# Performance work log

Hardware: AMD Instinct MI355X
Metric: run time of the kernel (lower is better)

The kernel has to match this reference:

```python
import jax, jax.numpy as jnp
import numpy as np

EMBED_DIM = 1024
NUM_HEADS = 16
HEAD_DIM = EMBED_DIM // NUM_HEADS


def setup_inputs() -> dict:
    key = jax.random.key(0)
    ks = jax.random.split(key, 12)
    B, S, D = 4, 2048, EMBED_DIM
    scale = 1.0 / np.sqrt(D)
    inp = {
        "query": jax.random.normal(ks[0], (B, S, D), jnp.float32),
        "key": jax.random.normal(ks[1], (B, S, D), jnp.float32),
        "value": jax.random.normal(ks[2], (B, S, D), jnp.float32),
        # nn.Linear weights: [out_features, in_features], y = x @ W.T + b
        "Wq": jax.random.normal(ks[3], (D, D), jnp.float32) * scale,
        "bq": jnp.zeros((D,), jnp.float32),
        "Wk": jax.random.normal(ks[4], (D, D), jnp.float32) * scale,
        "bk": jnp.zeros((D,), jnp.float32),
        "Wv": jax.random.normal(ks[5], (D, D), jnp.float32) * scale,
        "bv": jnp.zeros((D,), jnp.float32),
        "Wo": jax.random.normal(ks[6], (D, D), jnp.float32) * scale,
        "bo": jnp.zeros((D,), jnp.float32),
    }
    return inp


def reference(query, key, value, Wq, bq, Wk, bk, Wv, bv, Wo, bo):
    B, Sq, D = query.shape
    Sk = key.shape[1]
    H, Dh = NUM_HEADS, HEAD_DIM

    def proj(x, W, b):
        # [B,S,D] -> [B,H,S,Dh]
        y = jnp.einsum('bsd,ed->bse', x, W) + b
        return y.reshape(x.shape[0], x.shape[1], H, Dh).transpose(0, 2, 1, 3)

    q = proj(query, Wq, bq)
    k = proj(key, Wk, bk)
    v = proj(value, Wv, bv)

    # sigmoid attention (no softmax); dropout is identity in eval mode
    scores = jnp.einsum('bhqd,bhkd->bhqk', q, k) / jnp.sqrt(jnp.float32(Dh)).astype(q.dtype)
    attn = jax.nn.sigmoid(scores)
    out = jnp.einsum('bhqk,bhkd->bhqd', attn, v)

    out = out.transpose(0, 2, 1, 3).reshape(B, Sq, D)
    return jnp.einsum('bsd,ed->bse', out, Wo) + bo
```

## Files before the change

### kernel.cpp

```cpp
#include <hip/hip_runtime.h>


typedef _Float16 f16x2 __attribute__((ext_vector_type(2)));
typedef _Float16 f16x4 __attribute__((ext_vector_type(4)));
typedef _Float16 f16x8 __attribute__((ext_vector_type(8)));
typedef __fp16   h16x2 __attribute__((ext_vector_type(2)));
typedef float    f32x4 __attribute__((ext_vector_type(4)));
typedef float    f32x16 __attribute__((ext_vector_type(16)));

typedef __attribute__((address_space(3))) void* lds_vp;
typedef const __attribute__((address_space(1))) void* gbl_vp;

__device__ __forceinline__ void gld_lds16(const void* g, void* l) {
  __builtin_amdgcn_global_load_lds((gbl_vp)g, (lds_vp)l, 16, 0, 0);
}

__device__ __forceinline__ f16x8 cvt8(float4 a, float4 b) {
  return (f16x8){(_Float16)a.x, (_Float16)a.y, (_Float16)a.z, (_Float16)a.w,
                 (_Float16)b.x, (_Float16)b.y, (_Float16)b.z, (_Float16)b.w};
}

__device__ __forceinline__ f16x2 pk2(float a, float b) {
  h16x2 r = __builtin_amdgcn_cvt_pkrtz(a, b);
  return __builtin_bit_cast(f16x2, r);
}

__device__ __forceinline__ float exp2_fast(float x) {
#if __has_builtin(__builtin_amdgcn_exp2f)
  return __builtin_amdgcn_exp2f(x);
#else
  float r;
  asm("v_exp_f32 %0, %1" : "=v"(r) : "v"(x));
  return r;
#endif
}

#define BM 128
#define BN 128
#define BK 32

template <bool AF16, bool BF16, bool TRANSV, bool OUTF32, bool SWZ>
__global__ __launch_bounds__(256) void gemm_bt(const void* __restrict__ Av,
                                               const void* __restrict__ Bv,
                                               const float* __restrict__ bias,
                                               void* __restrict__ Yv,
                                               int M, int N, int K) {
  __shared__ __align__(16) _Float16 sA[BM * BK];
  __shared__ __align__(16) _Float16 sB[BN * BK];

  const int t = threadIdx.x, lane = t & 63, wid = t >> 6;
  int m0, n0;
  if constexpr (SWZ) {
    const int li = (int)(blockIdx.x + 64 * blockIdx.y);
    const int mb = (li & 7) * 8 + ((li >> 3) & 7);
    const int nb = li >> 6;
    m0 = mb * BM; n0 = nb * BN;
  } else {
    m0 = blockIdx.x * BM; n0 = blockIdx.y * BN;
  }
  const int wm = (wid >> 1) * 64, wn = (wid & 1) * 64;
  const int lrow = lane & 15, g = lane >> 4;

  f32x4 acc[4][4] = {};

  const int arow = 16 * wid + (lane >> 2);
  const int gq = (lane & 3) ^ ((lane >> 3) & 3);
  _Float16* lA1 = sA + wid * 512;
  _Float16* lA2 = sA + 2048 + wid * 512;
  _Float16* lB1 = sB + wid * 512;
  _Float16* lB2 = sB + 2048 + wid * 512;

  const int mrow = t >> 1, mhalf = t & 1;
  const int mm = (mrow >> 1) & 3;
  const int ch_lo = mrow * 4 + ((2 * mhalf) ^ mm);
  const int ch_hi = ch_lo ^ 1;

  const _Float16* pA16a = nullptr; const _Float16* pA16b = nullptr;
  const float* pA32 = nullptr;
  if constexpr (AF16) {
    const _Float16* A = (const _Float16*)Av;
    pA16a = A + (size_t)(m0 + arow) * K + gq * 8;
    pA16b = A + (size_t)(m0 + 64 + arow) * K + gq * 8;
  } else {
    pA32 = (const float*)Av + (size_t)(m0 + mrow) * K + mhalf * 16;
  }
  const _Float16* pB16a = nullptr; const _Float16* pB16b = nullptr;
  const float* pB32 = nullptr;
  if constexpr (BF16) {
    const _Float16* B = (const _Float16*)Bv;
    pB16a = B + (size_t)(n0 + arow) * K + gq * 8;
    pB16b = B + (size_t)(n0 + 64 + arow) * K + gq * 8;
  } else {
    pB32 = (const float*)Bv + (size_t)(n0 + mrow) * K + mhalf * 16;
  }

  const int xr = g ^ ((lrow >> 1) & 3);

  for (int k0 = 0; k0 < K; k0 += BK) {
    float4 av[4], bv4[4];
    if constexpr (!AF16) {
      const float4* p = (const float4*)(pA32 + k0);
      av[0] = p[0]; av[1] = p[1]; av[2] = p[2]; av[3] = p[3];
    }
    if constexpr (!BF16) {
      const float4* p = (const float4*)(pB32 + k0);
      bv4[0] = p[0]; bv4[1] = p[1]; bv4[2] = p[2]; bv4[3] = p[3];
    }
    __syncthreads();
    if constexpr (AF16) {
      gld_lds16(pA16a + k0, lA1);
      gld_lds16(pA16b + k0, lA2);
    } else {
      *(f16x8*)(sA + ch_lo * 8) = cvt8(av[0], av[1]);
      *(f16x8*)(sA + ch_hi * 8) = cvt8(av[2], av[3]);
    }
    if constexpr (BF16) {
      gld_lds16(pB16a + k0, lB1);
      gld_lds16(pB16b + k0, lB2);
    } else {
      *(f16x8*)(sB + ch_lo * 8) = cvt8(bv4[0], bv4[1]);
      *(f16x8*)(sB + ch_hi * 8) = cvt8(bv4[2], bv4[3]);
    }
    __syncthreads();

    f16x8 af[4], bf[4];
#pragma unroll
    for (int i = 0; i < 4; i++)
      af[i] = *(const f16x8*)(sA + (wm + i * 16 + lrow) * 32 + xr * 8);
#pragma unroll
    for (int j = 0; j < 4; j++)
      bf[j] = *(const f16x8*)(sB + (wn + j * 16 + lrow) * 32 + xr * 8);
#pragma unroll
    for (int i = 0; i < 4; i++)
#pragma unroll
      for (int j = 0; j < 4; j++)
        acc[i][j] = __builtin_amdgcn_mfma_f32_16x16x32_f16(af[i], bf[j], acc[i][j], 0, 0, 0);
  }

  const int orow = g * 4, ocol = lrow;
#pragma unroll
  for (int j = 0; j < 4; j++) {
    const int col = n0 + wn + j * 16 + ocol;
    const float bv = bias[col];
#pragma unroll
    for (int i = 0; i < 4; i++) {
      const int row = m0 + wm + i * 16 + orow;
      if constexpr (TRANSV) {
        _Float16* VT = (_Float16*)Yv;
        int s = row & 2047;
        int sp = (s & ~12) | ((s & 4) << 1) | ((s & 8) >> 1);
        _Float16* dst = VT + (((size_t)(row >> 11) * 16 + (col >> 6)) * 64 + (col & 63)) * 2048 + sp;
        f16x4 v = {(_Float16)(acc[i][j][0] + bv), (_Float16)(acc[i][j][1] + bv),
                   (_Float16)(acc[i][j][2] + bv), (_Float16)(acc[i][j][3] + bv)};
        *(f16x4*)dst = v;
      } else if constexpr (OUTF32) {
        float* Y = (float*)Yv;
#pragma unroll
        for (int r = 0; r < 4; r++) Y[(size_t)(row + r) * N + col] = acc[i][j][r] + bv;
      } else {
        _Float16* Y = (_Float16*)Yv;
#pragma unroll
        for (int r = 0; r < 4; r++) Y[(size_t)(row + r) * N + col] = (_Float16)(acc[i][j][r] + bv);
      }
    }
  }
}

__global__ __launch_bounds__(256) void qkv_gemm(const _Float16* __restrict__ Xq,
                                                const _Float16* __restrict__ Xk,
                                                const _Float16* __restrict__ Xv,
                                                const _Float16* __restrict__ W,
                                                const float* __restrict__ bq,
                                                const float* __restrict__ bk,
                                                const float* __restrict__ bv,
                                                _Float16* __restrict__ Qo,
                                                _Float16* __restrict__ Ko,
                                                _Float16* __restrict__ VT) {
  __shared__ __align__(16) _Float16 sA[BM * BK];
  __shared__ __align__(16) _Float16 sB[BN * BK];

  const int t = threadIdx.x, lane = t & 63, wid = t >> 6;
  const int li = (int)(blockIdx.x + 24 * blockIdx.y);
  const int xcol = li >> 6;
  const int mb = (li & 7) * 8 + ((li >> 3) & 7);
  const int n0g = xcol * BN, m0 = mb * BM;
  const int seg = xcol >> 3, n0 = n0g & 1023;
  const _Float16* A = (seg == 0) ? Xq : (seg == 1) ? Xk : Xv;
  const float* bias = (seg == 0) ? bq : (seg == 1) ? bk : bv;
  const int K = 1024;

  const int wm = (wid >> 1) * 64, wn = (wid & 1) * 64;
  const int lrow = lane & 15, g = lane >> 4;

  f32x4 acc[4][4] = {};

  const int arow = 16 * wid + (lane >> 2);
  const int gq = (lane & 3) ^ ((lane >> 3) & 3);
  _Float16* lA1 = sA + wid * 512;
  _Float16* lA2 = sA + 2048 + wid * 512;
  _Float16* lB1 = sB + wid * 512;
  _Float16* lB2 = sB + 2048 + wid * 512;

  const _Float16* pA16a = A + (size_t)(m0 + arow) * K + gq * 8;
  const _Float16* pA16b = A + (size_t)(m0 + 64 + arow) * K + gq * 8;
  const _Float16* pB16a = W + (size_t)(n0g + arow) * K + gq * 8;
  const _Float16* pB16b = W + (size_t)(n0g + 64 + arow) * K + gq * 8;

  const int xr = g ^ ((lrow >> 1) & 3);

  for (int k0 = 0; k0 < K; k0 += BK) {
    __syncthreads();
    gld_lds16(pA16a + k0, lA1);
    gld_lds16(pA16b + k0, lA2);
    gld_lds16(pB16a + k0, lB1);
    gld_lds16(pB16b + k0, lB2);
    __syncthreads();

    f16x8 af[4], bf[4];
#pragma unroll
    for (int i = 0; i < 4; i++)
      af[i] = *(const f16x8*)(sA + (wm + i * 16 + lrow) * 32 + xr * 8);
#pragma unroll
    for (int j = 0; j < 4; j++)
      bf[j] = *(const f16x8*)(sB + (wn + j * 16 + lrow) * 32 + xr * 8);
#pragma unroll
    for (int i = 0; i < 4; i++)
#pragma unroll
      for (int j = 0; j < 4; j++)
        acc[i][j] = __builtin_amdgcn_mfma_f32_16x16x32_f16(af[i], bf[j], acc[i][j], 0, 0, 0);
  }

  const int orow = g * 4, ocol = lrow;
#pragma unroll
  for (int j = 0; j < 4; j++) {
    const int col = n0 + wn + j * 16 + ocol;
    const float bvv = bias[col];
#pragma unroll
    for (int i = 0; i < 4; i++) {
      const int row = m0 + wm + i * 16 + orow;
      if (seg == 2) {
        int s = row & 2047;
        int sp = (s & ~12) | ((s & 4) << 1) | ((s & 8) >> 1);
        _Float16* dst = VT + (((size_t)(row >> 11) * 16 + (col >> 6)) * 64 + (col & 63)) * 2048 + sp;
        f16x4 v = {(_Float16)(acc[i][j][0] + bvv), (_Float16)(acc[i][j][1] + bvv),
                   (_Float16)(acc[i][j][2] + bvv), (_Float16)(acc[i][j][3] + bvv)};
        *(f16x4*)dst = v;
      } else {
        _Float16* Y = (seg == 0) ? Qo : Ko;
#pragma unroll
        for (int r = 0; r < 4; r++) Y[(size_t)(row + r) * 1024 + col] = (_Float16)(acc[i][j][r] + bvv);
      }
    }
  }
}

#define LDS_ROW 72
#define TILE_E (64 * LDS_ROW)

__global__ __launch_bounds__(256, 2) void attn_sig(const _Float16* __restrict__ Q,
                                                   const _Float16* __restrict__ K,
                                                   const _Float16* __restrict__ VT,
                                                   _Float16* __restrict__ O) {
  __shared__ __align__(16) _Float16 smem[4 * TILE_E];

  const int t = threadIdx.x, lane = t & 63, wid = t >> 6;
  const int l31 = lane & 31, g5 = lane >> 5;
  const int li = (int)(blockIdx.x + 8 * blockIdx.y + 128 * blockIdx.z);
  const int swz = (li & 7) * 64 + (li >> 3);
  const int qb = swz & 7, hb = swz >> 3;
  const int h = hb & 15, b = hb >> 4;
  const int q0 = qb * 256;
  const int qw = q0 + wid * 64;
  const int NT = 32;

  f16x8 qf0[4], qf1[4];
  {
    const _Float16* qp = Q + (size_t)(b * 2048 + qw + l31) * 1024 + h * 64;
#pragma unroll
    for (int dhc = 0; dhc < 4; dhc++) {
      qf0[dhc] = *(const f16x8*)(qp + dhc * 16 + g5 * 8) * (_Float16)-0.18033688f;
      qf1[dhc] = *(const f16x8*)(qp + 32 * 1024 + dhc * 16 + g5 * 8) * (_Float16)-0.18033688f;
    }
  }

  f32x16 oacc00 = {}, oacc01 = {}, oacc10 = {}, oacc11 = {};

  const int srow = t >> 2, scol = (t & 3) * 16;
  const _Float16* kbase = K + ((size_t)(b * 2048) + srow) * 1024 + h * 64 + scol;
  const _Float16* vbase = VT + ((size_t)((b * 16 + h) * 64 + srow)) * 2048 + scol;

#define LOAD_TILE(tile)                                                  \
  ka = *(const uint4*)(kbase + (size_t)(tile) * 64 * 1024);              \
  kb = *(const uint4*)(kbase + (size_t)(tile) * 64 * 1024 + 8);          \
  va = *(const uint4*)(vbase + (tile) * 64);                             \
  vb = *(const uint4*)(vbase + (tile) * 64 + 8);

#define WRITE_TILE(p)                                                    \
  {                                                                      \
    _Float16* dK = smem + (p) * 2 * TILE_E;                              \
    _Float16* dV = dK + TILE_E;                                          \
    *(uint4*)&dK[srow * LDS_ROW + scol] = ka;                            \
    *(uint4*)&dK[srow * LDS_ROW + scol + 8] = kb;                        \
    *(uint4*)&dV[srow * LDS_ROW + scol] = va;                            \
    *(uint4*)&dV[srow * LDS_ROW + scol + 8] = vb;                        \
  }

#define PACK_PF(pf, sacc)                                                \
  {                                                                      \
    _Pragma("unroll")                                                    \
    for (int G = 0; G < 2; G++) {                                        \
      union { f16x8 v; f16x2 hh[4]; } u;                                 \
      _Pragma("unroll")                                                  \
      for (int pr = 0; pr < 4; pr++) {                                   \
        float e0 = exp2_fast(sacc[G * 8 + pr * 2 + 0]);                  \
        float e1 = exp2_fast(sacc[G * 8 + pr * 2 + 1]);                  \
        u.hh[pr] = pk2(__builtin_amdgcn_rcpf(1.0f + e0),                 \
                       __builtin_amdgcn_rcpf(1.0f + e1));                \
      }                                                                  \
      pf[G] = u.v;                                                       \
    }                                                                    \
  }

#define CHUNK(c)                                                                      \
  {                                                                                   \
    const _Float16* sk_ = sKp + ((c) * 32 + l31) * LDS_ROW + g5 * 8;                  \
    f16x8 kf0 = *(const f16x8*)(sk_ + 0);                                             \
    f16x8 kf1 = *(const f16x8*)(sk_ + 16);                                            \
    f16x8 kf2 = *(const f16x8*)(sk_ + 32);                                            \
    f16x8 kf3 = *(const f16x8*)(sk_ + 48);                                            \
    f32x16 s0 = {}, s1 = {};                                                          \
    __builtin_amdgcn_s_setprio(1);                                                    \
    s0 = __builtin_amdgcn_mfma_f32_32x32x16_f16(kf0, qf0[0], s0, 0, 0, 0);            \
    s1 = __builtin_amdgcn_mfma_f32_32x32x16_f16(kf0, qf1[0], s1, 0, 0, 0);            \
    s0 = __builtin_amdgcn_mfma_f32_32x32x16_f16(kf1, qf0[1], s0, 0, 0, 0);            \
    s1 = __builtin_amdgcn_mfma_f32_32x32x16_f16(kf1, qf1[1], s1, 0, 0, 0);            \
    s0 = __builtin_amdgcn_mfma_f32_32x32x16_f16(kf2, qf0[2], s0, 0, 0, 0);            \
    s1 = __builtin_amdgcn_mfma_f32_32x32x16_f16(kf2, qf1[2], s1, 0, 0, 0);            \
    s0 = __builtin_amdgcn_mfma_f32_32x32x16_f16(kf3, qf0[3], s0, 0, 0, 0);            \
    s1 = __builtin_amdgcn_mfma_f32_32x32x16_f16(kf3, qf1[3], s1, 0, 0, 0);            \
    __builtin_amdgcn_s_setprio(0);                                                    \
    f16x8 pf0[2], pf1[2];                                                             \
    PACK_PF(pf0, s0);                                                                 \
    PACK_PF(pf1, s1);                                                                 \
    const _Float16* sv_ = sVp + l31 * LDS_ROW + (c) * 32 + g5 * 8;                    \
    f16x8 vf00 = *(const f16x8*)(sv_ + 0);                                            \
    f16x8 vf01 = *(const f16x8*)(sv_ + 16);                                           \
    f16x8 vf10 = *(const f16x8*)(sv_ + 32 * LDS_ROW);                                 \
    f16x8 vf11 = *(const f16x8*)(sv_ + 32 * LDS_ROW + 16);                            \
    __builtin_amdgcn_s_setprio(1);                                                    \
    oacc00 = __builtin_amdgcn_mfma_f32_32x32x16_f16(vf00, pf0[0], oacc00, 0, 0, 0);   \
    oacc10 = __builtin_amdgcn_mfma_f32_32x32x16_f16(vf00, pf1[0], oacc10, 0, 0, 0);   \
    oacc01 = __builtin_amdgcn_mfma_f32_32x32x16_f16(vf10, pf0[0], oacc01, 0, 0, 0);   \
    oacc11 = __builtin_amdgcn_mfma_f32_32x32x16_f16(vf10, pf1[0], oacc11, 0, 0, 0);   \
    oacc00 = __builtin_amdgcn_mfma_f32_32x32x16_f16(vf01, pf0[1], oacc00, 0, 0, 0);   \
    oacc10 = __builtin_amdgcn_mfma_f32_32x32x16_f16(vf01, pf1[1], oacc10, 0, 0, 0);   \
    oacc01 = __builtin_amdgcn_mfma_f32_32x32x16_f16(vf11, pf0[1], oacc01, 0, 0, 0);   \
    oacc11 = __builtin_amdgcn_mfma_f32_32x32x16_f16(vf11, pf1[1], oacc11, 0, 0, 0);   \
    __builtin_amdgcn_s_setprio(0);                                                    \
  }

  uint4 ka, kb, va, vb;

  LOAD_TILE(0);
  WRITE_TILE(0);
  LOAD_TILE(1);

  for (int tt = 0; tt < NT; ++tt) {
    const int p = tt & 1;
    const _Float16* sKp = smem + p * 2 * TILE_E;
    const _Float16* sVp = sKp + TILE_E;
    __syncthreads();
    if (tt + 1 < NT) { WRITE_TILE(p ^ 1); }
    if (tt + 2 < NT) { LOAD_TILE(tt + 2); }
    CHUNK(0);
    CHUNK(1);
  }

  _Float16* ep = smem;
#pragma unroll
  for (int pass = 0; pass < 2; pass++) {
    __syncthreads();
    if ((wid >> 1) == pass) {
      const int rbase = (wid & 1) * 64;
#pragma unroll
      for (int c = 0; c < 4; c++) {
        f16x4 a0 = {(_Float16)oacc00[4 * c + 0], (_Float16)oacc00[4 * c + 1],
                    (_Float16)oacc00[4 * c + 2], (_Float16)oacc00[4 * c + 3]};
        f16x4 a1 = {(_Float16)oacc01[4 * c + 0], (_Float16)oacc01[4 * c + 1],
                    (_Float16)oacc01[4 * c + 2], (_Float16)oacc01[4 * c + 3]};
        *(f16x4*)&ep[(rbase + l31) * LDS_ROW + 0 * 32 + c * 8 + g5 * 4] = a0;
        *(f16x4*)&ep[(rbase + l31) * LDS_ROW + 1 * 32 + c * 8 + g5 * 4] = a1;
        f16x4 b0 = {(_Float16)oacc10[4 * c + 0], (_Float16)oacc10[4 * c + 1],
                    (_Float16)oacc10[4 * c + 2], (_Float16)oacc10[4 * c + 3]};
        f16x4 b1 = {(_Float16)oacc11[4 * c + 0], (_Float16)oacc11[4 * c + 1],
                    (_Float16)oacc11[4 * c + 2], (_Float16)oacc11[4 * c + 3]};
        *(f16x4*)&ep[(rbase + 32 + l31) * LDS_ROW + 0 * 32 + c * 8 + g5 * 4] = b0;
        *(f16x4*)&ep[(rbase + 32 + l31) * LDS_ROW + 1 * 32 + c * 8 + g5 * 4] = b1;
      }
    }
    __syncthreads();
#pragma unroll
    for (int i = 0; i < 4; i++) {
      const int q = i * 32 + (t >> 3), dhc = t & 7;
      f16x8 row = *(const f16x8*)&ep[q * LDS_ROW + dhc * 8];
      *(f16x8*)(O + (size_t)(b * 2048 + q0 + pass * 128 + q) * 1024 + h * 64 + dhc * 8) = row;
    }
  }
#undef LOAD_TILE
#undef WRITE_TILE
#undef PACK_PF
#undef CHUNK
}

struct CvtArgs {
  const float* src[7];
  _Float16* dst[7];
  int n[7];
  int cnt;
};

__global__ __launch_bounds__(256) void cvt_f32_f16(CvtArgs a) {
  const int ti = blockIdx.y;
  if (ti >= a.cnt) return;
  const int i = (blockIdx.x * 256 + threadIdx.x) * 8;
  if (i >= a.n[ti]) return;
  const float4* s = (const float4*)(a.src[ti] + i);
  float4 x = s[0], y = s[1];
  *(f16x8*)(a.dst[ti] + i) = cvt8(x, y);
}

extern "C" void kernel_launch(void* const* d_in, const int* in_sizes, int n_in,
                              void* d_out, int out_size, void* d_ws, size_t ws_size,
                              hipStream_t stream) {
  const float* query = (const float*)d_in[0];
  const float* key   = (const float*)d_in[1];
  const float* value = (const float*)d_in[2];
  const float* Wq = (const float*)d_in[3];
  const float* bq = (const float*)d_in[4];
  const float* Wk = (const float*)d_in[5];
  const float* bk = (const float*)d_in[6];
  const float* Wv = (const float*)d_in[7];
  const float* bv = (const float*)d_in[8];
  const float* Wo = (const float*)d_in[9];
  const float* bo = (const float*)d_in[10];
  float* out = (float*)d_out;

  const int D = 1024, M = 8192;
  const size_t MB = 1024 * 1024;
  char* ws = (char*)d_ws;
  dim3 bb(256);

  if (ws_size >= 104 * MB) {
    _Float16* Xq = (_Float16*)(ws + 0 * MB);
    _Float16* Xk = (_Float16*)(ws + 16 * MB);
    _Float16* Xv = (_Float16*)(ws + 32 * MB);
    _Float16* Qp = (_Float16*)(ws + 48 * MB);
    _Float16* Kp = (_Float16*)(ws + 64 * MB);
    _Float16* VT = (_Float16*)(ws + 80 * MB);
    _Float16* Wf = (_Float16*)(ws + 96 * MB);
    _Float16* AO = Xq;
    CvtArgs ca{};
    ca.src[0] = query; ca.dst[0] = Xq; ca.n[0] = M * D;
    ca.src[1] = key;   ca.dst[1] = Xk; ca.n[1] = M * D;
    ca.src[2] = value; ca.dst[2] = Xv; ca.n[2] = M * D;
    ca.src[3] = Wq; ca.dst[3] = Wf + 0 * 1048576; ca.n[3] = D * D;
    ca.src[4] = Wk; ca.dst[4] = Wf + 1 * 1048576; ca.n[4] = D * D;
    ca.src[5] = Wv; ca.dst[5] = Wf + 2 * 1048576; ca.n[5] = D * D;
    ca.src[6] = Wo; ca.dst[6] = Wf + 3 * 1048576; ca.n[6] = D * D;
    ca.cnt = 7;
    cvt_f32_f16<<<dim3(4096, 7), bb, 0, stream>>>(ca);
    qkv_gemm<<<dim3(24, 64), bb, 0, stream>>>(Xq, Xk, Xv, Wf, bq, bk, bv, Qp, Kp, VT);
    attn_sig<<<dim3(8, 16, 4), bb, 0, stream>>>(Qp, Kp, VT, AO);
    gemm_bt<true, true, false, true, true><<<dim3(64, 8), bb, 0, stream>>>(AO, Wf + 3 * 1048576, bo, out, M, D, D);
  } else {
    _Float16* Qp = (_Float16*)(ws + 0 * MB);
    _Float16* Kp = (_Float16*)(ws + 16 * MB);
    _Float16* VT = (_Float16*)(ws + 32 * MB);
    _Float16* AO = (_Float16*)(ws + 48 * MB);
    gemm_bt<false, false, false, false, false><<<dim3(64, 8), bb, 0, stream>>>(query, Wq, bq, Qp, M, D, D);
    gemm_bt<false, false, false, false, false><<<dim3(64, 8), bb, 0, stream>>>(key,   Wk, bk, Kp, M, D, D);
    gemm_bt<false, false, true,  false, false><<<dim3(64, 8), bb, 0, stream>>>(value, Wv, bv, VT, M, D, D);
    attn_sig<<<dim3(8, 16, 4), bb, 0, stream>>>(Qp, Kp, VT, AO);
    gemm_bt<true, false, false, true, false><<<dim3(64, 8), bb, 0, stream>>>(AO, Wo, bo, out, M, D, D);
  }
}
```

Baseline: 349.6 us.

## Double GEMM K-tile to 64, fold Q scale into Wq conversion, flatten cvt grid

```diff
diff --git a/kernel.cpp b/kernel.cpp
--- a/kernel.cpp
+++ b/kernel.cpp
@@ -10,6 +10,8 @@
 
 typedef __attribute__((address_space(3))) void* lds_vp;
 typedef const __attribute__((address_space(1))) void* gbl_vp;
+
+#define QSCALE -0.18033688f
 
 __device__ __forceinline__ void gld_lds16(const void* g, void* l) {
   __builtin_amdgcn_global_load_lds((gbl_vp)g, (lds_vp)l, 16, 0, 0);
@@ -37,7 +39,7 @@
 
 #define BM 128
 #define BN 128
-#define BK 32
+#define BK 64
 
 template <bool AF16, bool BF16, bool TRANSV, bool OUTF32, bool SWZ>
 __global__ __launch_bounds__(256) void gemm_bt(const void* __restrict__ Av,
@@ -63,78 +65,78 @@
 
   f32x4 acc[4][4] = {};
 
-  const int arow = 16 * wid + (lane >> 2);
-  const int gq = (lane & 3) ^ ((lane >> 3) & 3);
-  _Float16* lA1 = sA + wid * 512;
-  _Float16* lA2 = sA + 2048 + wid * 512;
-  _Float16* lB1 = sB + wid * 512;
-  _Float16* lB2 = sB + 2048 + wid * 512;
+  const int srow8 = wid * 8 + (lane >> 3);
+  const int sgq = ((lane & 7) ^ (lane >> 3)) * 8;
 
   const int mrow = t >> 1, mhalf = t & 1;
-  const int mm = (mrow >> 1) & 3;
-  const int ch_lo = mrow * 4 + ((2 * mhalf) ^ mm);
-  const int ch_hi = ch_lo ^ 1;
-
-  const _Float16* pA16a = nullptr; const _Float16* pA16b = nullptr;
+
+  const _Float16* pAa = nullptr;
   const float* pA32 = nullptr;
   if constexpr (AF16) {
-    const _Float16* A = (const _Float16*)Av;
-    pA16a = A + (size_t)(m0 + arow) * K + gq * 8;
-    pA16b = A + (size_t)(m0 + 64 + arow) * K + gq * 8;
+    pAa = (const _Float16*)Av + (size_t)(m0 + srow8) * K + sgq;
   } else {
-    pA32 = (const float*)Av + (size_t)(m0 + mrow) * K + mhalf * 16;
-  }
-  const _Float16* pB16a = nullptr; const _Float16* pB16b = nullptr;
+    pA32 = (const float*)Av + (size_t)(m0 + mrow) * K + mhalf * 32;
+  }
+  const _Float16* pBa = nullptr;
   const float* pB32 = nullptr;
   if constexpr (BF16) {
-    const _Float16* B = (const _Float16*)Bv;
-    pB16a = B + (size_t)(n0 + arow) * K + gq * 8;
-    pB16b = B + (size_t)(n0 + 64 + arow) * K + gq * 8;
+    pBa = (const _Float16*)Bv + (size_t)(n0 + srow8) * K + sgq;
   } else {
-    pB32 = (const float*)Bv + (size_t)(n0 + mrow) * K + mhalf * 16;
-  }
-
-  const int xr = g ^ ((lrow >> 1) & 3);
+    pB32 = (const float*)Bv + (size_t)(n0 + mrow) * K + mhalf * 32;
+  }
 
   for (int k0 = 0; k0 < K; k0 += BK) {
-    float4 av[4], bv4[4];
+    float4 av[8], bv8[8];
     if constexpr (!AF16) {
       const float4* p = (const float4*)(pA32 + k0);
-      av[0] = p[0]; av[1] = p[1]; av[2] = p[2]; av[3] = p[3];
+#pragma unroll
+      for (int q = 0; q < 8; q++) av[q] = p[q];
     }
     if constexpr (!BF16) {
       const float4* p = (const float4*)(pB32 + k0);
-      bv4[0] = p[0]; bv4[1] = p[1]; bv4[2] = p[2]; bv4[3] = p[3];
+#pragma unroll
+      for (int q = 0; q < 8; q++) bv8[q] = p[q];
     }
     __syncthreads();
     if constexpr (AF16) {
-      gld_lds16(pA16a + k0, lA1);
-      gld_lds16(pA16b + k0, lA2);
+#pragma unroll
+      for (int i = 0; i < 4; i++)
+        gld_lds16(pAa + (size_t)i * 32 * K + k0, sA + i * 2048 + wid * 512);
     } else {
-      *(f16x8*)(sA + ch_lo * 8) = cvt8(av[0], av[1]);
-      *(f16x8*)(sA + ch_hi * 8) = cvt8(av[2], av[3]);
+#pragma unroll
+      for (int q = 0; q < 4; q++) {
+        const int glog = mhalf * 4 + q;
+        *(f16x8*)(sA + mrow * 64 + (glog ^ (mrow & 7)) * 8) = cvt8(av[2 * q], av[2 * q + 1]);
+      }
     }
     if constexpr (BF16) {
-      gld_lds16(pB16a + k0, lB1);
-      gld_lds16(pB16b + k0, lB2);
+#pragma unroll
+      for (int i = 0; i < 4; i++)
+        gld_lds16(pBa + (size_t)i * 32 * K + k0, sB + i * 2048 + wid * 512);
     } else {
-      *(f16x8*)(sB + ch_lo * 8) = cvt8(bv4[0], bv4[1]);
-      *(f16x8*)(sB + ch_hi * 8) = cvt8(bv4[2], bv4[3]);
-    }
-    __syncthreads();
-
-    f16x8 af[4], bf[4];
-#pragma unroll
-    for (int i = 0; i < 4; i++)
-      af[i] = *(const f16x8*)(sA + (wm + i * 16 + lrow) * 32 + xr * 8);
-#pragma unroll
-    for (int j = 0; j < 4; j++)
-      bf[j] = *(const f16x8*)(sB + (wn + j * 16 + lrow) * 32 + xr * 8);
-#pragma unroll
-    for (int i = 0; i < 4; i++)
+#pragma unroll
+      for (int q = 0; q < 4; q++) {
+        const int glog = mhalf * 4 + q;
+        *(f16x8*)(sB + mrow * 64 + (glog ^ (mrow & 7)) * 8) = cvt8(bv8[2 * q], bv8[2 * q + 1]);
+      }
+    }
+    __syncthreads();
+
+#pragma unroll
+    for (int kc = 0; kc < 2; kc++) {
+      f16x8 af[4], bf[4];
+#pragma unroll
+      for (int i = 0; i < 4; i++)
+        af[i] = *(const f16x8*)(sA + (wm + i * 16 + lrow) * 64 + ((kc * 4 + g) ^ (lrow & 7)) * 8);
 #pragma unroll
       for (int j = 0; j < 4; j++)
-        acc[i][j] = __builtin_amdgcn_mfma_f32_16x16x32_f16(af[i], bf[j], acc[i][j], 0, 0, 0);
+        bf[j] = *(const f16x8*)(sB + (wn + j * 16 + lrow) * 64 + ((kc * 4 + g) ^ (lrow & 7)) * 8);
+#pragma unroll
+      for (int i = 0; i < 4; i++)
+#pragma unroll
+        for (int j = 0; j < 4; j++)
+          acc[i][j] = __builtin_amdgcn_mfma_f32_16x16x32_f16(af[i], bf[j], acc[i][j], 0, 0, 0);
+    }
   }
 
   const int orow = g * 4, ocol = lrow;
@@ -187,6 +189,7 @@
   const int seg = xcol >> 3, n0 = n0g & 1023;
   const _Float16* A = (seg == 0) ? Xq : (seg == 1) ? Xk : Xv;
   const float* bias = (seg == 0) ? bq : (seg == 1) ? bk : bv;
+  const float bscale = (seg == 0) ? QSCALE : 1.0f;
   const int K = 1024;
 
   const int wm = (wid >> 1) * 64, wn = (wid & 1) * 64;
@@ -194,47 +197,44 @@
 
   f32x4 acc[4][4] = {};
 
-  const int arow = 16 * wid + (lane >> 2);
-  const int gq = (lane & 3) ^ ((lane >> 3) & 3);
-  _Float16* lA1 = sA + wid * 512;
-  _Float16* lA2 = sA + 2048 + wid * 512;
-  _Float16* lB1 = sB + wid * 512;
-  _Float16* lB2 = sB + 2048 + wid * 512;
-
-  const _Float16* pA16a = A + (size_t)(m0 + arow) * K + gq * 8;
-  const _Float16* pA16b = A + (size_t)(m0 + 64 + arow) * K + gq * 8;
-  const _Float16* pB16a = W + (size_t)(n0g + arow) * K + gq * 8;
-  const _Float16* pB16b = W + (size_t)(n0g + 64 + arow) * K + gq * 8;
-
-  const int xr = g ^ ((lrow >> 1) & 3);
+  const int srow8 = wid * 8 + (lane >> 3);
+  const int sgq = ((lane & 7) ^ (lane >> 3)) * 8;
+
+  const _Float16* pAa = A + (size_t)(m0 + srow8) * K + sgq;
+  const _Float16* pBa = W + (size_t)(n0g + srow8) * K + sgq;
 
   for (int k0 = 0; k0 < K; k0 += BK) {
     __syncthreads();
-    gld_lds16(pA16a + k0, lA1);
-    gld_lds16(pA16b + k0, lA2);
-    gld_lds16(pB16a + k0, lB1);
-    gld_lds16(pB16b + k0, lB2);
-    __syncthreads();
-
-    f16x8 af[4], bf[4];
 #pragma unroll
     for (int i = 0; i < 4; i++)
-      af[i] = *(const f16x8*)(sA + (wm + i * 16 + lrow) * 32 + xr * 8);
-#pragma unroll
-    for (int j = 0; j < 4; j++)
-      bf[j] = *(const f16x8*)(sB + (wn + j * 16 + lrow) * 32 + xr * 8);
+      gld_lds16(pAa + (size_t)i * 32 * K + k0, sA + i * 2048 + wid * 512);
 #pragma unroll
     for (int i = 0; i < 4; i++)
+      gld_lds16(pBa + (size_t)i * 32 * K + k0, sB + i * 2048 + wid * 512);
+    __syncthreads();
+
+#pragma unroll
+    for (int kc = 0; kc < 2; kc++) {
+      f16x8 af[4], bf[4];
+#pragma unroll
+      for (int i = 0; i < 4; i++)
+        af[i] = *(const f16x8*)(sA + (wm + i * 16 + lrow) * 64 + ((kc * 4 + g) ^ (lrow & 7)) * 8);
 #pragma unroll
       for (int j = 0; j < 4; j++)
-        acc[i][j] = __builtin_amdgcn_mfma_f32_16x16x32_f16(af[i], bf[j], acc[i][j], 0, 0, 0);
+        bf[j] = *(const f16x8*)(sB + (wn + j * 16 + lrow) * 64 + ((kc * 4 + g) ^ (lrow & 7)) * 8);
+#pragma unroll
+      for (int i = 0; i < 4; i++)
+#pragma unroll
+        for (int j = 0; j < 4; j++)
+          acc[i][j] = __builtin_amdgcn_mfma_f32_16x16x32_f16(af[i], bf[j], acc[i][j], 0, 0, 0);
+    }
   }
 
   const int orow = g * 4, ocol = lrow;
 #pragma unroll
   for (int j = 0; j < 4; j++) {
     const int col = n0 + wn + j * 16 + ocol;
-    const float bvv = bias[col];
+    const float bvv = bias[col] * bscale;
 #pragma unroll
     for (int i = 0; i < 4; i++) {
       const int row = m0 + wm + i * 16 + orow;
@@ -257,6 +257,7 @@
 #define LDS_ROW 72
 #define TILE_E (64 * LDS_ROW)
 
+template <bool SCALEQ>
 __global__ __launch_bounds__(256, 2) void attn_sig(const _Float16* __restrict__ Q,
                                                    const _Float16* __restrict__ K,
                                                    const _Float16* __restrict__ VT,
@@ -278,8 +279,13 @@
     const _Float16* qp = Q + (size_t)(b * 2048 + qw + l31) * 1024 + h * 64;
 #pragma unroll
     for (int dhc = 0; dhc < 4; dhc++) {
-      qf0[dhc] = *(const f16x8*)(qp + dhc * 16 + g5 * 8) * (_Float16)-0.18033688f;
-      qf1[dhc] = *(const f16x8*)(qp + 32 * 1024 + dhc * 16 + g5 * 8) * (_Float16)-0.18033688f;
+      if constexpr (SCALEQ) {
+        qf0[dhc] = *(const f16x8*)(qp + dhc * 16 + g5 * 8) * (_Float16)QSCALE;
+        qf1[dhc] = *(const f16x8*)(qp + 32 * 1024 + dhc * 16 + g5 * 8) * (_Float16)QSCALE;
+      } else {
+        qf0[dhc] = *(const f16x8*)(qp + dhc * 16 + g5 * 8);
+        qf1[dhc] = *(const f16x8*)(qp + 32 * 1024 + dhc * 16 + g5 * 8);
+      }
     }
   }
 
@@ -420,13 +426,24 @@
 };
 
 __global__ __launch_bounds__(256) void cvt_f32_f16(CvtArgs a) {
-  const int ti = blockIdx.y;
-  if (ti >= a.cnt) return;
-  const int i = (blockIdx.x * 256 + threadIdx.x) * 8;
-  if (i >= a.n[ti]) return;
-  const float4* s = (const float4*)(a.src[ti] + i);
+  const int id = blockIdx.x * 256 + threadIdx.x;
+  int ti, off;
+  if (id < 3 * 1048576) {
+    ti = id >> 20;
+    off = (id & 1048575) * 8;
+  } else {
+    const int w = id - 3 * 1048576;
+    ti = 3 + (w >> 17);
+    off = (w & 131071) * 8;
+  }
+  const float4* s = (const float4*)(a.src[ti] + off);
   float4 x = s[0], y = s[1];
-  *(f16x8*)(a.dst[ti] + i) = cvt8(x, y);
+  if (ti == 3) {
+    const float qs = QSCALE;
+    x.x *= qs; x.y *= qs; x.z *= qs; x.w *= qs;
+    y.x *= qs; y.y *= qs; y.z *= qs; y.w *= qs;
+  }
+  *(f16x8*)(a.dst[ti] + off) = cvt8(x, y);
 }
 
 extern "C" void kernel_launch(void* const* d_in, const int* in_sizes, int n_in,
@@ -468,9 +485,9 @@
     ca.src[5] = Wv; ca.dst[5] = Wf + 2 * 1048576; ca.n[5] = D * D;
     ca.src[6] = Wo; ca.dst[6] = Wf + 3 * 1048576; ca.n[6] = D * D;
     ca.cnt = 7;
-    cvt_f32_f16<<<dim3(4096, 7), bb, 0, stream>>>(ca);
+    cvt_f32_f16<<<dim3(14336), bb, 0, stream>>>(ca);
     qkv_gemm<<<dim3(24, 64), bb, 0, stream>>>(Xq, Xk, Xv, Wf, bq, bk, bv, Qp, Kp, VT);
-    attn_sig<<<dim3(8, 16, 4), bb, 0, stream>>>(Qp, Kp, VT, AO);
+    attn_sig<false><<<dim3(8, 16, 4), bb, 0, stream>>>(Qp, Kp, VT, AO);
     gemm_bt<true, true, false, true, true><<<dim3(64, 8), bb, 0, stream>>>(AO, Wf + 3 * 1048576, bo, out, M, D, D);
   } else {
     _Float16* Qp = (_Float16*)(ws + 0 * MB);
@@ -480,7 +497,7 @@
     gemm_bt<false, false, false, false, false><<<dim3(64, 8), bb, 0, stream>>>(query, Wq, bq, Qp, M, D, D);
     gemm_bt<false, false, false, false, false><<<dim3(64, 8), bb, 0, stream>>>(key,   Wk, bk, Kp, M, D, D);
     gemm_bt<false, false, true,  false, false><<<dim3(64, 8), bb, 0, stream>>>(value, Wv, bv, VT, M, D, D);
-    attn_sig<<<dim3(8, 16, 4), bb, 0, stream>>>(Qp, Kp, VT, AO);
+    attn_sig<true><<<dim3(8, 16, 4), bb, 0, stream>>>(Qp, Kp, VT, AO);
     gemm_bt<true, false, false, true, false><<<dim3(64, 8), bb, 0, stream>>>(AO, Wo, bo, out, M, D, D);
   }
 }
```

After: 327.6 us. 1.07x faster.
